# Kernel optimization log

Hardware: AMD Instinct MI355X
Metric: run time of the kernel (lower is better)

## Reference

```python
import jax, jax.numpy as jnp
import numpy as np

# --- configuration (mirrors VFNet cfg) ---
B, NC = 1, 6                     # batch, surround cameras
C_IN, H_F, W_F = 64, 44, 80      # fused feature level (height//8, width//8)
XD, YD, ZD = 100, 100, 20        # voxel dims (x forward, inverse-depth spaced)
X0, X1 = 2.0, 51.5
Y0, Y1 = -25.0, 24.5
Z0, Z1 = -3.0, 2.7
DB, D_STR, D_END = 50, 2.0, 50.0 # projection depth bins (inverse-depth spaced)
VDIM, FOUT = 64, 256             # voxel_pre_dim, feat_out_dim
P = H_F * W_F
EPS = 1e-8


def _axes():
    ego_x = 1.0 / jnp.linspace(1.0 / X1, 1.0 / X0, XD)[::-1]  # ascending, nonuniform
    ego_y = jnp.linspace(Y0, Y1, YD)
    ego_z = jnp.linspace(Z0, Z1, ZD)
    return ego_x, ego_y, ego_z


def _voxel_pts():
    ex, ey, ez = _axes()
    gz, gy, gx = jnp.meshgrid(ez, ey, ex, indexing='ij')      # [Z,Y,X]
    pts = jnp.stack([gx, gy, gz], 0).reshape(3, -1)
    return jnp.concatenate([pts, jnp.ones((1, pts.shape[1]), pts.dtype)], 0)  # [4,N]


def _bilinear2d(img, u, v):
    C, H, W = img.shape
    u0, v0 = jnp.floor(u), jnp.floor(v)
    du, dv = u - u0, v - v0
    u0i = jnp.clip(u0.astype(jnp.int32), 0, W - 1); u1i = jnp.clip(u0i + 1, 0, W - 1)
    v0i = jnp.clip(v0.astype(jnp.int32), 0, H - 1); v1i = jnp.clip(v0i + 1, 0, H - 1)
    g = lambda vi, ui: img[:, vi, ui]
    return (g(v0i, u0i) * (1 - du) * (1 - dv) + g(v0i, u1i) * du * (1 - dv)
            + g(v1i, u0i) * (1 - du) * dv + g(v1i, u1i) * du * dv)


def _nonuniform_index(axis, q):
    # searchsorted + in-bin lerp: metric coord -> continuous index on nonuniform axis
    qc = jnp.clip(q, axis[0], axis[-1] - 1e-6)
    k = jnp.clip(jnp.searchsorted(axis, qc, side='left') - 1, 0, axis.shape[0] - 2)
    t = (qc - axis[k]) / (axis[k + 1] - axis[k] + 1e-12)
    return k.astype(qc.dtype) + t


def _trilinear(vol, xi, yi, zi):
    Cc, Zz, Yy, Xx = vol.shape
    def sp(i, n):
        i0 = jnp.floor(i); t = i - i0
        a = jnp.clip(i0.astype(jnp.int32), 0, n - 1)
        return a, jnp.clip(a + 1, 0, n - 1), t
    x0, x1, tx = sp(xi, Xx); y0, y1, ty = sp(yi, Yy); z0, z1, tz = sp(zi, Zz)
    g = lambda z, y, x: vol[:, z, y, x]
    c0 = (g(z0, y0, x0) * (1 - tx) + g(z0, y0, x1) * tx) * (1 - ty) + (g(z0, y1, x0) * (1 - tx) + g(z0, y1, x1) * tx) * ty
    c1 = (g(z1, y0, x0) * (1 - tx) + g(z1, y0, x1) * tx) * (1 - ty) + (g(z1, y1, x0) * (1 - tx) + g(z1, y1, x1) * tx) * ty
    return c0 * (1 - tz) + c1 * tz


def _conv2d(x, w, b):
    y = jax.lax.conv_general_dilated(x, w, (1, 1), 'SAME', dimension_numbers=('NCHW', 'OIHW', 'NCHW'))
    return y + b[None, :, None, None]


def _conv3d(x, w, b):
    y = jax.lax.conv_general_dilated(x, w, (1, 1, 1), 'SAME', dimension_numbers=('NCDHW', 'OIDHW', 'NCDHW'))
    return y + b[None, :, None, None, None]


def _forward(feats, masks, K, ext, w_ov, b_ov, w_no, b_no, w_fu, b_fu, w_r1, b_r1, w_r2, b_r2):
    ex, ey, ez = _axes()
    vpts = _voxel_pts()                                        # [4,N]
    fm = jnp.concatenate([feats[0], masks[0]], axis=1)         # [NC, C+1, H, W]
    ext_inv = jnp.linalg.inv(ext)

    # --- backproject surround-view features into the nonuniform voxel grid ---
    def per_cam(img, Kc, Ei):
        pix = Kc @ (Ei @ vpts)
        z = pix[2]
        u = pix[0] / (z + EPS); v = pix[1] / (z + EPS)
        valid = (z > EPS) & (u >= 0) & (u <= W_F - 1) & (v >= 0) & (v <= H_F - 1)
        return _bilinear2d(img, u, v) * valid, valid.astype(img.dtype)

    s, valid = jax.vmap(per_cam)(fm, K, ext_inv)               # [NC,C+1,N], [NC,N]
    count = valid.sum(0)
    cat = jnp.concatenate([s[:3].sum(0), s[3:].sum(0)], axis=0)  # [2*(C+1),N]
    ov = jax.nn.elu(w_ov @ cat + b_ov[:, None]) * (count == 2)
    no = jax.nn.elu(w_no @ s.sum(0) + b_no[:, None]) * (count == 1)
    vf = (ov + no).reshape(VDIM, ZD, YD, XD)                   # [64,Z,Y,X]

    # --- nonuniform-x -> uniform-x remap (searchsorted + lerp) + conv3d fusion ---
    xi_axis = _nonuniform_index(ex, jnp.linspace(X0, X1, XD))
    ZI, YI, XI = jnp.meshgrid(jnp.arange(ZD, dtype=vf.dtype), jnp.arange(YD, dtype=vf.dtype), xi_axis, indexing='ij')
    vf_remap = _trilinear(vf, XI, YI, ZI)
    vol = jax.nn.elu(_conv3d(jnp.concatenate([vf, vf_remap], 0)[None], w_fu, b_fu))[0]  # [64,Z,Y,X]

    # --- project fused voxel features into each camera frustum over inv-depth bins ---
    uu, vv = jnp.meshgrid(jnp.arange(W_F), jnp.arange(H_F), indexing='xy')
    pix_grid = jnp.stack([uu.reshape(-1).astype(feats.dtype), vv.reshape(-1).astype(feats.dtype), jnp.ones((P,), feats.dtype)], 0)  # [3,P]
    dbins = 1.0 / jnp.linspace(1.0 / D_END, 1.0 / D_STR, DB)[::-1]  # ascending, inv-depth spaced
    K3inv = jnp.linalg.inv(K[:, :3, :3])

    def per_cam_proj(Ki, Ec):
        dirs = Ki @ pix_grid                                   # [3,P]
        pc = dirs[:, None, :] * dbins[None, :, None]           # [3,D,P]
        pc = jnp.concatenate([pc, jnp.ones((1, DB, P), pc.dtype)], 0)
        pw = (Ec @ pc.reshape(4, -1)).reshape(4, DB, P)        # ego-frame points
        wx, wy, wz = pw[0], pw[1], pw[2]
        xi = _nonuniform_index(ex, wx)
        yi = (wy - Y0) / (Y1 - Y0) * (YD - 1)
        zi = (wz - Z0) / (Z1 - Z0) * (ZD - 1)
        inb = (wx >= X0) & (wx <= X1) & (yi >= 0) & (yi <= YD - 1) & (zi >= 0) & (zi <= ZD - 1)
        samp = _trilinear(vol, xi, yi, zi) * inb               # [64,D,P]
        return samp.reshape(VDIM * DB, H_F, W_F)

    proj = jax.vmap(per_cam_proj)(K3inv, ext)                  # [NC, 64*D, H, W]
    h = jax.nn.elu(_conv2d(proj, w_r1, b_r1))
    return jax.nn.elu(_conv2d(h, w_r2, b_r2))                  # [NC, 256, H, W]


def setup_inputs() -> dict:
    key = jax.random.key(0)
    ks = jax.random.split(key, 8)
    feats = jax.random.normal(ks[0], (B, NC, C_IN, H_F, W_F), jnp.float32)
    masks = jnp.ones((B, NC, 1, H_F, W_F), jnp.float32)
    Kn = np.eye(4, dtype=np.float32)
    Kn[0, 0] = Kn[1, 1] = 40.0; Kn[0, 2] = 40.0; Kn[1, 2] = 22.0  # ~90deg hfov at 80px
    K = np.tile(Kn, (NC, 1, 1))
    ext = np.zeros((NC, 4, 4), dtype=np.float32)
    for i in range(NC):
        th = 2 * np.pi * i / NC
        c, s0 = np.cos(th), np.sin(th)
        R = np.array([[s0, 0, c], [-c, 0, s0], [0, -1, 0]], dtype=np.float32)  # cam(right,down,fwd)->ego
        ext[i, :3, :3] = R
        ext[i, :3, 3] = np.array([c, s0, 0.8], dtype=np.float32)
        ext[i, 3, 3] = 1.0
    w_ov = jax.random.normal(ks[1], (VDIM, 2 * (C_IN + 1)), jnp.float32) / np.sqrt(2 * (C_IN + 1)).astype(np.float32)
    w_no = jax.random.normal(ks[2], (VDIM, C_IN + 1), jnp.float32) / np.sqrt(C_IN + 1).astype(np.float32)
    w_fu = jax.random.normal(ks[3], (VDIM, 2 * VDIM, 3, 3, 3), jnp.float32) / np.sqrt(2 * VDIM * 27).astype(np.float32)
    w_r1 = jax.random.normal(ks[4], (FOUT, VDIM * DB, 3, 3), jnp.float32) / np.sqrt(VDIM * DB * 9).astype(np.float32)
    w_r2 = jax.random.normal(ks[5], (FOUT, FOUT, 3, 3), jnp.float32) / np.sqrt(FOUT * 9).astype(np.float32)
    z = lambda n: jnp.zeros((n,), jnp.float32)
    return {"feats": feats, "masks": masks, "K": jnp.asarray(K), "ext": jnp.asarray(ext),
            "w_ov": w_ov, "b_ov": z(VDIM), "w_no": w_no, "b_no": z(VDIM),
            "w_fu": w_fu, "b_fu": z(VDIM), "w_r1": w_r1, "b_r1": z(FOUT),
            "w_r2": w_r2, "b_r2": z(FOUT)}


def reference(feats, masks, K, ext, w_ov, b_ov, w_no, b_no, w_fu, b_fu, w_r1, b_r1, w_r2, b_r2):
    return _forward(feats, masks, K, ext, w_ov, b_ov, w_no, b_no, w_fu, b_fu, w_r1, b_r1, w_r2, b_r2)
```

## Files before the change

kernel.cpp:

```cpp
#include <hip/hip_runtime.h>
#include <math.h>

#define NCAM 6
#define CIN  64
#define HF   44
#define WF   80
#define PP   (HF*WF)
#define XD   100
#define YD   100
#define ZD   20
#define NVOX (XD*YD*ZD)
#define DBN  50
#define VDIM 64
#define FOUT 256
#define EPSF 1e-8f

typedef _Float16 f16x4 __attribute__((ext_vector_type(4)));
typedef _Float16 f16x8 __attribute__((ext_vector_type(8)));
typedef float    f32x4 __attribute__((ext_vector_type(4)));

#define OFF_KE    0
#define OFF_K3I   96
#define OFF_XI    160
#define OFF_DBIN  260
#define OFF_WOVT  320
#define OFF_WNOT  8640
#define B_VOL     51200UL
#define B_WT1     51200UL
#define B_H       14796800UL
#define B_VIN     25651200UL
#define B_PROJ    25651200UL
#define B_WT2     25651200UL
#define B_WT3     76851200UL

__device__ __forceinline__ float eluf(float x) { return x > 0.f ? x : expm1f(x); }

#define AX_A    (1.0f/51.5f)
#define AX_STEP ((0.5f - 1.0f/51.5f)/99.0f)

__device__ __forceinline__ void inv3x3(const float m[9], float o[9]) {
    float a00 = m[4]*m[8] - m[5]*m[7];
    float a10 = m[5]*m[6] - m[3]*m[8];
    float a20 = m[3]*m[7] - m[4]*m[6];
    float det = m[0]*a00 + m[1]*a10 + m[2]*a20;
    float id = 1.0f/det;
    o[0] = a00*id;
    o[1] = (m[2]*m[7] - m[1]*m[8])*id;
    o[2] = (m[1]*m[5] - m[2]*m[4])*id;
    o[3] = a10*id;
    o[4] = (m[0]*m[8] - m[2]*m[6])*id;
    o[5] = (m[2]*m[3] - m[0]*m[5])*id;
    o[6] = a20*id;
    o[7] = (m[1]*m[6] - m[0]*m[7])*id;
    o[8] = (m[0]*m[4] - m[1]*m[3])*id;
}

__global__ __launch_bounds__(256) void setup_kernel(const float* K, const float* ext,
                                                    const float* w_ov, const float* w_no,
                                                    float* ws) {
    int t = threadIdx.x;
    if (t < NCAM) {
        const float* E = ext + t*16;
        float R[9] = {E[0],E[1],E[2], E[4],E[5],E[6], E[8],E[9],E[10]};
        float Ri[9];
        inv3x3(R, Ri);
        float tx=E[3], ty=E[7], tz=E[11];
        float bx = -(Ri[0]*tx + Ri[1]*ty + Ri[2]*tz);
        float by = -(Ri[3]*tx + Ri[4]*ty + Ri[5]*tz);
        float bz = -(Ri[6]*tx + Ri[7]*ty + Ri[8]*tz);
        float Ei[16] = {Ri[0],Ri[1],Ri[2],bx, Ri[3],Ri[4],Ri[5],by, Ri[6],Ri[7],Ri[8],bz, 0,0,0,1};
        const float* Km = K + t*16;
        float* KE = ws + OFF_KE + t*16;
        for (int r=0;r<4;r++)
            for (int c=0;c<4;c++) {
                float s=0.f;
                for (int k=0;k<4;k++) s += Km[r*4+k]*Ei[k*4+c];
                KE[r*4+c]=s;
            }
        float Kr[9] = {Km[0],Km[1],Km[2], Km[4],Km[5],Km[6], Km[8],Km[9],Km[10]};
        float Ki[9];
        inv3x3(Kr, Ki);
        float* KI = ws + OFF_K3I + t*9;
        for (int i=0;i<9;i++) KI[i]=Ki[i];
    }
    if (t >= 64 && t < 64+XD) {
        int x = t-64;
        float ex0 = 1.0f/(AX_A + 99.0f*AX_STEP);
        float exN = 1.0f/AX_A;
        float q = 2.0f + (float)x * (49.5f/99.0f);
        float qc = fminf(fmaxf(q, ex0), exN - 1e-6f);
        float f = 99.0f - (1.0f/qc - AX_A)/AX_STEP;
        int k = min(max((int)floorf(f),0),98);
        float exk  = 1.0f/(AX_A + (float)(99-k)*AX_STEP);
        float exk1 = 1.0f/(AX_A + (float)(98-k)*AX_STEP);
        ws[OFF_XI + x] = (float)k + (qc - exk)/(exk1 - exk + 1e-12f);
    }
    if (t >= 192 && t < 192+DBN) {
        int d = t-192;
        float sa = 1.0f/50.0f;
        float ss = (0.5f - sa)/49.0f;
        ws[OFF_DBIN + d] = 1.0f/(sa + (float)(49-d)*ss);
    }
    for (int i = t; i < 130*64; i += 256) {
        int k = i >> 6, c = i & 63;
        ws[OFF_WOVT + i] = w_ov[c*130 + k];
    }
    for (int i = t; i < 65*64; i += 256) {
        int k = i >> 6, c = i & 63;
        ws[OFF_WNOT + i] = w_no[c*65 + k];
    }
}

__global__ __launch_bounds__(256) void tw1_kernel(const float* w, _Float16* o) {
    int idx = blockIdx.x*256 + threadIdx.x;
    int cp  = idx % 3200;
    int oc  = (idx/3200) & 255;
    int tap = idx/(3200*256);
    int d = cp >> 6, v = cp & 63;
    o[idx] = (_Float16)w[((size_t)oc*3200 + v*50 + d)*9 + tap];
}
__global__ __launch_bounds__(256) void tw2_kernel(const float* w, _Float16* o) {
    int idx = blockIdx.x*256 + threadIdx.x;
    int ic  = idx & 255;
    int oc  = (idx >> 8) & 255;
    int tap = idx >> 16;
    o[idx] = (_Float16)w[((size_t)oc*256 + ic)*9 + tap];
}
__global__ __launch_bounds__(256) void tw3_kernel(const float* w, _Float16* o) {
    int idx = blockIdx.x*256 + threadIdx.x;
    int ci  = idx & 127;
    int oc  = (idx >> 7) & 63;
    int tap = idx >> 13;
    o[idx] = (_Float16)w[((size_t)oc*128 + ci)*27 + tap];
}

__global__ __launch_bounds__(256) void backproject_kernel(const float* feats, const float* masks,
                                                          const float* ws,
                                                          const float* b_ov, const float* b_no,
                                                          _Float16* vin) {
    int wave = threadIdx.x >> 6;
    int lane = threadIdx.x & 63;
    int n = blockIdx.x*4 + wave;
    int x = n % XD;
    int y = (n / XD) % YD;
    int z = n / (XD*YD);
    float gx = 1.0f/(AX_A + (float)(99-x)*AX_STEP);
    float gy = -25.0f + (float)y * (49.5f/99.0f);
    float gz = -3.0f  + (float)z * (5.7f/19.0f);

    float sA = 0.f, sB = 0.f, sA64 = 0.f, sB64 = 0.f;
    int cnt = 0;
    for (int cam = 0; cam < NCAM; ++cam) {
        const float* KE = ws + OFF_KE + cam*16;
        float px = KE[0]*gx + KE[1]*gy + KE[2]*gz + KE[3];
        float py = KE[4]*gx + KE[5]*gy + KE[6]*gz + KE[7];
        float pz = KE[8]*gx + KE[9]*gy + KE[10]*gz + KE[11];
        float inv = 1.0f/(pz + EPSF);
        float u = px*inv, v = py*inv;
        bool valid = (pz > EPSF) && (u >= 0.f) && (u <= 79.f) && (v >= 0.f) && (v <= 43.f);
        if (valid) {
            cnt++;
            float u0 = floorf(u), v0 = floorf(v);
            float du = u-u0, dv = v-v0;
            int u0i = min(max((int)u0,0),WF-1), u1i = min(u0i+1,WF-1);
            int v0i = min(max((int)v0,0),HF-1), v1i = min(v0i+1,HF-1);
            float w00=(1.f-du)*(1.f-dv), w01=du*(1.f-dv), w10=(1.f-du)*dv, w11=du*dv;
            int i00=v0i*WF+u0i, i01=v0i*WF+u1i, i10=v1i*WF+u0i, i11=v1i*WF+u1i;
            const float* img = feats + (cam*CIN + lane)*PP;
            float val = w00*img[i00] + w01*img[i01] + w10*img[i10] + w11*img[i11];
            const float* mg = masks + cam*PP;
            float mv = w00*mg[i00] + w01*mg[i01] + w10*mg[i10] + w11*mg[i11];
            if (cam < 3) { sA += val; sA64 += mv; }
            else         { sB += val; sB64 += mv; }
        }
    }
    float out = 0.f;
    if (cnt == 2) {
        const float* wT = ws + OFF_WOVT;
        float acc = b_ov[lane];
        for (int k = 0; k < 64; ++k) {
            float ca = __shfl(sA, k, 64);
            float cb = __shfl(sB, k, 64);
            acc += wT[k*64 + lane]*ca + wT[(65+k)*64 + lane]*cb;
        }
        acc += wT[64*64 + lane]*sA64 + wT[129*64 + lane]*sB64;
        out = eluf(acc);
    } else if (cnt == 1) {
        const float* wT = ws + OFF_WNOT;
        float s = sA + sB, s64 = sA64 + sB64;
        float acc = b_no[lane];
        for (int k = 0; k < 64; ++k) {
            float ca = __shfl(s, k, 64);
            acc += wT[k*64 + lane]*ca;
        }
        acc += wT[64*64 + lane]*s64;
        out = eluf(acc);
    }
    vin[(size_t)n*128 + lane] = (_Float16)out;
}

__global__ __launch_bounds__(256) void remap_kernel(const float* ws, _Float16* vin) {
    int wave = threadIdx.x >> 6, lane = threadIdx.x & 63;
    int n = blockIdx.x*4 + wave;
    int x = n % XD;
    float xi = ws[OFF_XI + x];
    float fx = floorf(xi);
    float t = xi - fx;
    int x0 = min(max((int)fx,0),XD-1);
    int x1 = min(x0+1, XD-1);
    size_t rowb = (size_t)(n - x)*128;
    float r = (float)vin[rowb + (size_t)x0*128 + lane]*(1.f-t)
            + (float)vin[rowb + (size_t)x1*128 + lane]*t;
    vin[(size_t)n*128 + 64 + lane] = (_Float16)r;
}

__global__ __launch_bounds__(256,1) void conv3d_mfma_kernel(const _Float16* __restrict__ vin,
                                                            const _Float16* __restrict__ wT,
                                                            const float* __restrict__ bias,
                                                            _Float16* __restrict__ vol) {
    __shared__ __align__(16) _Float16 Bs[9*104*40];
    int tid = threadIdx.x, lane = tid & 63, wave = tid >> 6;
    int ln = lane & 15, kq = lane >> 4;
    int y = blockIdx.x % 100, z = blockIdx.x / 100;
    int nt0 = wave*2;
    int ntn = (wave == 3) ? 1 : 2;
    f32x4 zero4 = {0.f,0.f,0.f,0.f};
    f32x4 acc[4][2];
    for (int i=0;i<4;i++) for (int t=0;t<2;t++) acc[i][t] = zero4;

    for (int c0 = 0; c0 < 128; c0 += 32) {
        __syncthreads();
        for (int g = tid; g < 9*104*4; g += 256) {
            int ic8 = g & 3;
            int xe  = (g >> 2) % 104;
            int rid = g / (104*4);
            int xx = xe - 1, yy = y + rid%3 - 1, zz = z + rid/3 - 1;
            f16x8 val = {0,0,0,0,0,0,0,0};
            if (xx >= 0 && xx < 100 && yy >= 0 && yy < 100 && zz >= 0 && zz < 20)
                val = *(const f16x8*)(vin + (size_t)((zz*100 + yy)*100 + xx)*128 + c0 + ic8*8);
            *(f16x8*)(&Bs[(rid*104 + xe)*40 + ic8*8]) = val;
        }
        __syncthreads();
        for (int tap = 0; tap < 27; ++tap) {
            int dx = tap % 3, rid = tap / 3;
            const _Float16* wp = wT + (size_t)tap*64*128 + c0 + kq*8;
            f16x8 a0 = *(const f16x8*)(wp + (ln+ 0)*128);
            f16x8 a1 = *(const f16x8*)(wp + (ln+16)*128);
            f16x8 a2 = *(const f16x8*)(wp + (ln+32)*128);
            f16x8 a3 = *(const f16x8*)(wp + (ln+48)*128);
            for (int t = 0; t < ntn; ++t) {
                int xe = min(16*(nt0+t) + ln + dx, 103);
                f16x8 b = *(const f16x8*)(&Bs[(rid*104 + xe)*40 + kq*8]);
                acc[0][t] = __builtin_amdgcn_mfma_f32_16x16x32_f16(a0, b, acc[0][t], 0,0,0);
                acc[1][t] = __builtin_amdgcn_mfma_f32_16x16x32_f16(a1, b, acc[1][t], 0,0,0);
                acc[2][t] = __builtin_amdgcn_mfma_f32_16x16x32_f16(a2, b, acc[2][t], 0,0,0);
                acc[3][t] = __builtin_amdgcn_mfma_f32_16x16x32_f16(a3, b, acc[3][t], 0,0,0);
            }
        }
    }
    for (int i = 0; i < 4; ++i) {
        int oc0 = i*16 + kq*4;
        f32x4 bv = *(const f32x4*)(bias + oc0);
        for (int t = 0; t < ntn; ++t) {
            int x = 16*(nt0+t) + ln;
            if (x < 100) {
                size_t n = (size_t)(z*100 + y)*100 + x;
                f16x4 s;
                s[0] = (_Float16)eluf(acc[i][t][0] + bv[0]);
                s[1] = (_Float16)eluf(acc[i][t][1] + bv[1]);
                s[2] = (_Float16)eluf(acc[i][t][2] + bv[2]);
                s[3] = (_Float16)eluf(acc[i][t][3] + bv[3]);
                *(f16x4*)(vol + n*64 + oc0) = s;
            }
        }
    }
}

__global__ __launch_bounds__(256) void project_kernel(const float* ws, const float* ext,
                                                      const _Float16* vol, _Float16* proj) {
    __shared__ unsigned s_off[256][8];
    __shared__ float    s_w[256][8];
    int tid = threadIdx.x;
    int item = blockIdx.x*256 + tid;
    int d = item % 50;
    int p = (item/50) % 3520;
    int cam = item / (50*3520);
    {
        float uu = (float)(p % WF), vv = (float)(p / WF);
        const float* KI = ws + OFF_K3I + cam*9;
        float dxr = KI[0]*uu + KI[1]*vv + KI[2];
        float dyr = KI[3]*uu + KI[4]*vv + KI[5];
        float dzr = KI[6]*uu + KI[7]*vv + KI[8];
        float dep = ws[OFF_DBIN + d];
        float cx = dxr*dep, cy = dyr*dep, cz = dzr*dep;
        const float* E = ext + cam*16;
        float wx = E[0]*cx + E[1]*cy + E[2]*cz  + E[3];
        float wy = E[4]*cx + E[5]*cy + E[6]*cz  + E[7];
        float wz = E[8]*cx + E[9]*cy + E[10]*cz + E[11];
        float ex0 = 1.0f/(AX_A + 99.0f*AX_STEP);
        float exN = 1.0f/AX_A;
        float qc = fminf(fmaxf(wx, ex0), exN - 1e-6f);
        float f = 99.0f - (1.0f/qc - AX_A)/AX_STEP;
        int k = min(max((int)floorf(f),0),98);
        float exk  = 1.0f/(AX_A + (float)(99-k)*AX_STEP);
        float exk1 = 1.0f/(AX_A + (float)(98-k)*AX_STEP);
        float xi = (float)k + (qc - exk)/(exk1 - exk + 1e-12f);
        float yi = (wy + 25.0f) * (99.0f/49.5f);
        float zi = (wz + 3.0f)  * (19.0f/5.7f);
        float scale = ((wx >= 2.0f) && (wx <= 51.5f) && (yi >= 0.f) && (yi <= 99.f)
                       && (zi >= 0.f) && (zi <= 19.f)) ? 1.f : 0.f;
        float fx = floorf(xi), fy = floorf(yi), fz = floorf(zi);
        float tx = xi-fx, ty = yi-fy, tz = zi-fz;
        int x0 = min(max((int)fx,0),XD-1), x1 = min(x0+1,XD-1);
        int y0 = min(max((int)fy,0),YD-1), y1 = min(y0+1,YD-1);
        int z0 = min(max((int)fz,0),ZD-1), z1 = min(z0+1,ZD-1);
        s_off[tid][0] = (unsigned)(((z0*YD+y0)*XD+x0)*64); s_w[tid][0] = (1.f-tx)*(1.f-ty)*(1.f-tz)*scale;
        s_off[tid][1] = (unsigned)(((z0*YD+y0)*XD+x1)*64); s_w[tid][1] = tx*(1.f-ty)*(1.f-tz)*scale;
        s_off[tid][2] = (unsigned)(((z0*YD+y1)*XD+x0)*64); s_w[tid][2] = (1.f-tx)*ty*(1.f-tz)*scale;
        s_off[tid][3] = (unsigned)(((z0*YD+y1)*XD+x1)*64); s_w[tid][3] = tx*ty*(1.f-tz)*scale;
        s_off[tid][4] = (unsigned)(((z1*YD+y0)*XD+x0)*64); s_w[tid][4] = (1.f-tx)*(1.f-ty)*tz*scale;
        s_off[tid][5] = (unsigned)(((z1*YD+y0)*XD+x1)*64); s_w[tid][5] = tx*(1.f-ty)*tz*scale;
        s_off[tid][6] = (unsigned)(((z1*YD+y1)*XD+x0)*64); s_w[tid][6] = (1.f-tx)*ty*tz*scale;
        s_off[tid][7] = (unsigned)(((z1*YD+y1)*XD+x1)*64); s_w[tid][7] = tx*ty*tz*scale;
    }
    __syncthreads();
    int wave = tid >> 6, lane = tid & 63;
    size_t outbase = (size_t)blockIdx.x*256 + wave*64;
    for (int j = 0; j < 64; ++j) {
        int it = wave*64 + j;
        float a = 0.f;
        #pragma unroll
        for (int c = 0; c < 8; ++c)
            a += s_w[it][c] * (float)vol[s_off[it][c] + lane];
        proj[(outbase + j)*64 + lane] = (_Float16)a;
    }
}

template<int ICN, bool OUT16>
__global__ __launch_bounds__(256,2) void conv2d_mfma_kernel(const _Float16* __restrict__ in,
                                                            const _Float16* __restrict__ wT,
                                                            const float* __restrict__ bias,
                                                            void* __restrict__ outp) {
    __shared__ __align__(16) _Float16 Bs[4*82*40];
    int tid = threadIdx.x, lane = tid & 63, wave = tid >> 6;
    int wm = wave >> 1, wn = wave & 1;
    int ln = lane & 15, kq = lane >> 4;
    int bid = blockIdx.x;
    int ocq = bid & 3;
    int rest = bid >> 2;
    int cam = rest % 6;
    int h0 = (rest / 6)*2;
    int ocb = ocq*64 + wm*32;
    size_t campix0 = (size_t)cam*3520;
    f32x4 zero4 = {0.f,0.f,0.f,0.f};
    f32x4 acc[2][5];
    for (int i=0;i<2;i++) for (int t=0;t<5;t++) acc[i][t] = zero4;

    for (int c0 = 0; c0 < ICN; c0 += 32) {
        __syncthreads();
        for (int g = tid; g < 4*82*4; g += 256) {
            int ic8 = g & 3;
            int we  = (g >> 2) % 82;
            int re  = g / (82*4);
            int h = h0 - 1 + re;
            int w = we - 1;
            f16x8 val = {0,0,0,0,0,0,0,0};
            if (h >= 0 && h < HF && w >= 0 && w < WF)
                val = *(const f16x8*)(in + (campix0 + h*80 + w)*ICN + c0 + ic8*8);
            *(f16x8*)(&Bs[(re*82 + we)*40 + ic8*8]) = val;
        }
        __syncthreads();
        const _Float16* wbase = wT + (size_t)ocb*ICN + c0 + kq*8;
        f16x8 a0n = *(const f16x8*)(wbase + (size_t)(ln+ 0)*ICN);
        f16x8 a1n = *(const f16x8*)(wbase + (size_t)(ln+16)*ICN);
        #pragma unroll
        for (int tap = 0; tap < 9; ++tap) {
            f16x8 a0 = a0n, a1 = a1n;
            if (tap < 8) {
                const _Float16* wp = wbase + (size_t)(tap+1)*256*ICN;
                a0n = *(const f16x8*)(wp + (size_t)(ln+ 0)*ICN);
                a1n = *(const f16x8*)(wp + (size_t)(ln+16)*ICN);
            }
            int ky = tap/3, kx = tap%3;
            int rbase = (wn + ky)*82 + ln + kx;
            #pragma unroll
            for (int t = 0; t < 5; ++t) {
                f16x8 b = *(const f16x8*)(&Bs[(rbase + 16*t)*40 + kq*8]);
                acc[0][t] = __builtin_amdgcn_mfma_f32_16x16x32_f16(a0, b, acc[0][t], 0,0,0);
                acc[1][t] = __builtin_amdgcn_mfma_f32_16x16x32_f16(a1, b, acc[1][t], 0,0,0);
            }
        }
    }
    int pixrow = h0 + wn;
    for (int i = 0; i < 2; ++i) {
        int oc0 = ocb + i*16 + kq*4;
        f32x4 bv = *(const f32x4*)(bias + oc0);
        for (int t = 0; t < 5; ++t) {
            int pix = pixrow*80 + 16*t + ln;
            float v0 = eluf(acc[i][t][0] + bv[0]);
            float v1 = eluf(acc[i][t][1] + bv[1]);
            float v2 = eluf(acc[i][t][2] + bv[2]);
            float v3 = eluf(acc[i][t][3] + bv[3]);
            if (OUT16) {
                f16x4 s; s[0]=(_Float16)v0; s[1]=(_Float16)v1; s[2]=(_Float16)v2; s[3]=(_Float16)v3;
                *(f16x4*)((_Float16*)outp + (campix0 + pix)*256 + oc0) = s;
            } else {
                float* op = (float*)outp + ((size_t)(cam*256 + oc0))*PP + pix;
                op[0] = v0; op[PP] = v1; op[2*PP] = v2; op[3*PP] = v3;
            }
        }
    }
}

extern "C" void kernel_launch(void* const* d_in, const int* in_sizes, int n_in,
                              void* d_out, int out_size, void* d_ws, size_t ws_size,
                              hipStream_t stream) {
    const float* feats = (const float*)d_in[0];
    const float* masks = (const float*)d_in[1];
    const float* K     = (const float*)d_in[2];
    const float* ext   = (const float*)d_in[3];
    const float* w_ov  = (const float*)d_in[4];
    const float* b_ov  = (const float*)d_in[5];
    const float* w_no  = (const float*)d_in[6];
    const float* b_no  = (const float*)d_in[7];
    const float* w_fu  = (const float*)d_in[8];
    const float* b_fu  = (const float*)d_in[9];
    const float* w_r1  = (const float*)d_in[10];
    const float* b_r1  = (const float*)d_in[11];
    const float* w_r2  = (const float*)d_in[12];
    const float* b_r2  = (const float*)d_in[13];
    char* base = (char*)d_ws;
    float*    wsf  = (float*)base;
    _Float16* vol  = (_Float16*)(base + B_VOL);
    _Float16* wT1  = (_Float16*)(base + B_WT1);
    _Float16* h    = (_Float16*)(base + B_H);
    _Float16* vin  = (_Float16*)(base + B_VIN);
    _Float16* proj = (_Float16*)(base + B_PROJ);
    _Float16* wT2  = (_Float16*)(base + B_WT2);
    _Float16* wT3  = (_Float16*)(base + B_WT3);
    float* out = (float*)d_out;

    setup_kernel<<<1, 256, 0, stream>>>(K, ext, w_ov, w_no, wsf);
    tw3_kernel<<<(27*64*128)/256, 256, 0, stream>>>(w_fu, wT3);
    backproject_kernel<<<NVOX/4, 256, 0, stream>>>(feats, masks, wsf, b_ov, b_no, vin);
    remap_kernel<<<NVOX/4, 256, 0, stream>>>(wsf, vin);
    conv3d_mfma_kernel<<<ZD*YD, 256, 0, stream>>>(vin, wT3, b_fu, vol);
    project_kernel<<<(NCAM*PP*DBN)/256, 256, 0, stream>>>(wsf, ext, vol, proj);
    tw1_kernel<<<(9*256*3200)/256, 256, 0, stream>>>(w_r1, wT1);
    conv2d_mfma_kernel<3200, true><<<4*NCAM*22, 256, 0, stream>>>(proj, wT1, b_r1, h);
    tw2_kernel<<<(9*256*256)/256, 256, 0, stream>>>(w_r2, wT2);
    conv2d_mfma_kernel<256, false><<<4*NCAM*22, 256, 0, stream>>>(h, wT2, b_r2, out);
}
```

Before: 1.815 ms.

## Double-buffer conv2d input staging with register prefetch; prefetch conv3d weights

The conv2d kernel now uses two LDS buffers and register-staged global loads, so the next channel chunk is fetched while the current one is being computed. It also loads all nine tap weight fragments up front, which removes one barrier per chunk. The conv3d kernel gets software-prefetched weight fragments, a smaller LDS row stride (36 instead of 40) and launch bounds that allow two blocks per CU. In exchange, register pressure rises and the new padding may cause LDS bank conflicts.

```diff
diff --git a/kernel.cpp b/kernel.cpp
--- a/kernel.cpp
+++ b/kernel.cpp
@@ -214,11 +214,11 @@
     vin[(size_t)n*128 + 64 + lane] = (_Float16)r;
 }
 
-__global__ __launch_bounds__(256,1) void conv3d_mfma_kernel(const _Float16* __restrict__ vin,
+__global__ __launch_bounds__(256,2) void conv3d_mfma_kernel(const _Float16* __restrict__ vin,
                                                             const _Float16* __restrict__ wT,
                                                             const float* __restrict__ bias,
                                                             _Float16* __restrict__ vol) {
-    __shared__ __align__(16) _Float16 Bs[9*104*40];
+    __shared__ __align__(16) _Float16 Bs[9*104*36];
     int tid = threadIdx.x, lane = tid & 63, wave = tid >> 6;
     int ln = lane & 15, kq = lane >> 4;
     int y = blockIdx.x % 100, z = blockIdx.x / 100;
@@ -238,19 +238,27 @@
             f16x8 val = {0,0,0,0,0,0,0,0};
             if (xx >= 0 && xx < 100 && yy >= 0 && yy < 100 && zz >= 0 && zz < 20)
                 val = *(const f16x8*)(vin + (size_t)((zz*100 + yy)*100 + xx)*128 + c0 + ic8*8);
-            *(f16x8*)(&Bs[(rid*104 + xe)*40 + ic8*8]) = val;
+            *(f16x8*)(&Bs[(rid*104 + xe)*36 + ic8*8]) = val;
         }
         __syncthreads();
+        const _Float16* wp0 = wT + c0 + kq*8;
+        f16x8 a0n = *(const f16x8*)(wp0 + (ln+ 0)*128);
+        f16x8 a1n = *(const f16x8*)(wp0 + (ln+16)*128);
+        f16x8 a2n = *(const f16x8*)(wp0 + (ln+32)*128);
+        f16x8 a3n = *(const f16x8*)(wp0 + (ln+48)*128);
         for (int tap = 0; tap < 27; ++tap) {
+            f16x8 a0 = a0n, a1 = a1n, a2 = a2n, a3 = a3n;
+            if (tap < 26) {
+                const _Float16* wp = wT + (size_t)(tap+1)*64*128 + c0 + kq*8;
+                a0n = *(const f16x8*)(wp + (ln+ 0)*128);
+                a1n = *(const f16x8*)(wp + (ln+16)*128);
+                a2n = *(const f16x8*)(wp + (ln+32)*128);
+                a3n = *(const f16x8*)(wp + (ln+48)*128);
+            }
             int dx = tap % 3, rid = tap / 3;
-            const _Float16* wp = wT + (size_t)tap*64*128 + c0 + kq*8;
-            f16x8 a0 = *(const f16x8*)(wp + (ln+ 0)*128);
-            f16x8 a1 = *(const f16x8*)(wp + (ln+16)*128);
-            f16x8 a2 = *(const f16x8*)(wp + (ln+32)*128);
-            f16x8 a3 = *(const f16x8*)(wp + (ln+48)*128);
             for (int t = 0; t < ntn; ++t) {
                 int xe = min(16*(nt0+t) + ln + dx, 103);
-                f16x8 b = *(const f16x8*)(&Bs[(rid*104 + xe)*40 + kq*8]);
+                f16x8 b = *(const f16x8*)(&Bs[(rid*104 + xe)*36 + kq*8]);
                 acc[0][t] = __builtin_amdgcn_mfma_f32_16x16x32_f16(a0, b, acc[0][t], 0,0,0);
                 acc[1][t] = __builtin_amdgcn_mfma_f32_16x16x32_f16(a1, b, acc[1][t], 0,0,0);
                 acc[2][t] = __builtin_amdgcn_mfma_f32_16x16x32_f16(a2, b, acc[2][t], 0,0,0);
@@ -341,7 +349,9 @@
                                                             const _Float16* __restrict__ wT,
                                                             const float* __restrict__ bias,
                                                             void* __restrict__ outp) {
-    __shared__ __align__(16) _Float16 Bs[4*82*40];
+    constexpr int NCH = ICN/32;
+    constexpr int NSLOT = 6;
+    __shared__ __align__(16) _Float16 Bs[2][4*82*36];
     int tid = threadIdx.x, lane = tid & 63, wave = tid >> 6;
     int wm = wave >> 1, wn = wave & 1;
     int ln = lane & 15, kq = lane >> 4;
@@ -356,38 +366,65 @@
     f32x4 acc[2][5];
     for (int i=0;i<2;i++) for (int t=0;t<5;t++) acc[i][t] = zero4;
 
-    for (int c0 = 0; c0 < ICN; c0 += 32) {
-        __syncthreads();
-        for (int g = tid; g < 4*82*4; g += 256) {
+    size_t soff[NSLOT];
+    int    slds[NSLOT];
+    bool   sok[NSLOT];
+    #pragma unroll
+    for (int i = 0; i < NSLOT; ++i) {
+        int g = tid + i*256;
+        if (g < 4*82*4) {
             int ic8 = g & 3;
             int we  = (g >> 2) % 82;
             int re  = g / (82*4);
             int h = h0 - 1 + re;
             int w = we - 1;
-            f16x8 val = {0,0,0,0,0,0,0,0};
-            if (h >= 0 && h < HF && w >= 0 && w < WF)
-                val = *(const f16x8*)(in + (campix0 + h*80 + w)*ICN + c0 + ic8*8);
-            *(f16x8*)(&Bs[(re*82 + we)*40 + ic8*8]) = val;
-        }
+            sok[i]  = (h >= 0 && h < HF && w >= 0 && w < WF);
+            soff[i] = (campix0 + h*80 + w)*(size_t)ICN + ic8*8;
+            slds[i] = (re*82 + we)*36 + ic8*8;
+        } else { sok[i] = false; soff[i] = 0; slds[i] = -1; }
+    }
+
+    f16x8 sreg[NSLOT];
+    #pragma unroll
+    for (int i = 0; i < NSLOT; ++i) {
+        f16x8 v = {0,0,0,0,0,0,0,0};
+        if (sok[i]) v = *(const f16x8*)(in + soff[i]);
+        sreg[i] = v;
+    }
+
+    const _Float16* wbase0 = wT + (size_t)ocb*ICN + kq*8;
+    for (int c = 0; c < NCH; ++c) {
+        int buf = c & 1;
+        #pragma unroll
+        for (int i = 0; i < NSLOT; ++i)
+            if (slds[i] >= 0) *(f16x8*)(&Bs[buf][slds[i]]) = sreg[i];
         __syncthreads();
-        const _Float16* wbase = wT + (size_t)ocb*ICN + c0 + kq*8;
-        f16x8 a0n = *(const f16x8*)(wbase + (size_t)(ln+ 0)*ICN);
-        f16x8 a1n = *(const f16x8*)(wbase + (size_t)(ln+16)*ICN);
+        if (c + 1 < NCH) {
+            int c1 = (c+1)*32;
+            #pragma unroll
+            for (int i = 0; i < NSLOT; ++i) {
+                f16x8 v = {0,0,0,0,0,0,0,0};
+                if (sok[i]) v = *(const f16x8*)(in + soff[i] + c1);
+                sreg[i] = v;
+            }
+        }
+        f16x8 A0[9], A1[9];
+        const _Float16* wb = wbase0 + c*32;
         #pragma unroll
         for (int tap = 0; tap < 9; ++tap) {
-            f16x8 a0 = a0n, a1 = a1n;
-            if (tap < 8) {
-                const _Float16* wp = wbase + (size_t)(tap+1)*256*ICN;
-                a0n = *(const f16x8*)(wp + (size_t)(ln+ 0)*ICN);
-                a1n = *(const f16x8*)(wp + (size_t)(ln+16)*ICN);
-            }
+            const _Float16* wp = wb + (size_t)tap*256*ICN;
+            A0[tap] = *(const f16x8*)(wp + (size_t)(ln+ 0)*ICN);
+            A1[tap] = *(const f16x8*)(wp + (size_t)(ln+16)*ICN);
+        }
+        #pragma unroll
+        for (int tap = 0; tap < 9; ++tap) {
             int ky = tap/3, kx = tap%3;
             int rbase = (wn + ky)*82 + ln + kx;
             #pragma unroll
             for (int t = 0; t < 5; ++t) {
-                f16x8 b = *(const f16x8*)(&Bs[(rbase + 16*t)*40 + kq*8]);
-                acc[0][t] = __builtin_amdgcn_mfma_f32_16x16x32_f16(a0, b, acc[0][t], 0,0,0);
-                acc[1][t] = __builtin_amdgcn_mfma_f32_16x16x32_f16(a1, b, acc[1][t], 0,0,0);
+                f16x8 b = *(const f16x8*)(&Bs[buf][(rbase + 16*t)*36 + kq*8]);
+                acc[0][t] = __builtin_amdgcn_mfma_f32_16x16x32_f16(A0[tap], b, acc[0][t], 0,0,0);
+                acc[1][t] = __builtin_amdgcn_mfma_f32_16x16x32_f16(A1[tap], b, acc[1][t], 0,0,0);
             }
         }
     }
```

Result: faster. 1.753 ms (-3.4%).
